# Performance work log

Hardware: AMD Instinct MI355X
Metric: run time of the kernel (lower is better)

## Reference

```python
import jax, jax.numpy as jnp
import numpy as np
from jax import lax

B, S, D, H, T = 128, 512, 128, 128, 20


def setup_inputs() -> dict:
    key = jax.random.key(0)
    ks = jax.random.split(key, 16)
    sc = 1.0 / np.sqrt(H)
    u = lambda k, shape: jax.random.uniform(k, shape, jnp.float32, -sc, sc)
    return {
        "inputs": jax.random.normal(ks[0], (B, S, D), jnp.float32),
        "tags": jax.random.randint(ks[1], (B, S), 0, T),
        "mask": jnp.ones((B, S), jnp.bool_),
        "w_ih_f": u(ks[2], (4 * H, D)),
        "w_hh_f": u(ks[3], (4 * H, H)),
        "b_f": u(ks[4], (4 * H,)),
        "w_ih_b": u(ks[5], (4 * H, D)),
        "w_hh_b": u(ks[6], (4 * H, H)),
        "b_b": u(ks[7], (4 * H,)),
        "w_out": u(ks[8], (T, 2 * H)),
        "b_out": u(ks[9], (T,)),
        "start_trans": jax.random.uniform(ks[10], (T,), jnp.float32, -0.1, 0.1),
        "end_trans": jax.random.uniform(ks[11], (T,), jnp.float32, -0.1, 0.1),
        "trans": jax.random.uniform(ks[12], (T, T), jnp.float32, -0.1, 0.1),
    }


def _lstm_dir(x, w_ih, w_hh, b, reverse):
    # x: [B,S,D] -> hidden states [B,S,H]
    xp = jnp.einsum('bsd,gd->bsg', x, w_ih) + b  # precomputed input gates [B,S,4H]
    if reverse:
        xp = xp[:, ::-1]
    h0 = jnp.zeros((x.shape[0], H), x.dtype)
    c0 = jnp.zeros((x.shape[0], H), x.dtype)

    def step(carry, xt):
        h, c = carry
        g = xt + h @ w_hh.T
        i, f, gg, o = jnp.split(g, 4, axis=-1)
        i, f, o = jax.nn.sigmoid(i), jax.nn.sigmoid(f), jax.nn.sigmoid(o)
        c = f * c + i * jnp.tanh(gg)
        h = o * jnp.tanh(c)
        return (h, c), h

    _, hs = lax.scan(step, (h0, c0), xp.transpose(1, 0, 2))
    hs = hs.transpose(1, 0, 2)  # [B,S,H]
    if reverse:
        hs = hs[:, ::-1]
    return hs


def _crf_nll(em, tags, mask, start_trans, end_trans, trans):
    # em: [B,S,T]; torchcrf log-likelihood, reduction='mean', negated
    b, s, t = em.shape
    maskf = mask.astype(em.dtype)
    batch = jnp.arange(b)
    # numerator: score of the gold path
    num = start_trans[tags[:, 0]] + em[batch, 0, tags[:, 0]]
    em_tag = jnp.take_along_axis(em, tags[:, :, None], axis=2)[:, :, 0]  # [B,S]
    trans_tag = trans[tags[:, :-1], tags[:, 1:]]  # [B,S-1]
    num = num + jnp.sum((trans_tag + em_tag[:, 1:]) * maskf[:, 1:], axis=1)
    seq_ends = jnp.sum(mask.astype(jnp.int32), axis=1) - 1
    num = num + end_trans[tags[batch, seq_ends]]
    # denominator: forward algorithm (logsumexp semiring) via scan
    score0 = start_trans[None, :] + em[:, 0]  # [B,T]

    def step(score, inp):
        em_t, m_t = inp
        nxt = jax.nn.logsumexp(score[:, :, None] + trans[None] + em_t[:, None, :], axis=1)
        return jnp.where(m_t[:, None], nxt, score), None

    score, _ = lax.scan(step, score0, (em[:, 1:].transpose(1, 0, 2), mask[:, 1:].T))
    den = jax.nn.logsumexp(score + end_trans[None, :], axis=1)
    return -jnp.mean(num - den)


def reference(inputs, tags, mask, w_ih_f, w_hh_f, b_f, w_ih_b, w_hh_b, b_b,
              w_out, b_out, start_trans, end_trans, trans):
    h_f = _lstm_dir(inputs, w_ih_f, w_hh_f, b_f, reverse=False)
    h_b = _lstm_dir(inputs, w_ih_b, w_hh_b, b_b, reverse=True)
    lstm_out = jnp.concatenate([h_f, h_b], axis=-1)  # [B,S,2H]
    emissions = jnp.einsum('bsh,th->bst', lstm_out, w_out) + b_out  # [B,S,T]
    return _crf_nll(emissions, tags, mask, start_trans, end_trans, trans)
```

## Files before the change

### kernel.cpp

```cpp
#include <hip/hip_runtime.h>
#include <cstdint>
#include <cstddef>

#define DEVINL __device__ __forceinline__

constexpr int Bz = 128, Sl = 512, Dm = 128, Hd = 128, NC = 1024, Tt = 20;
constexpr int Mrows = Bz * Sl;

constexpr size_t OFF_XP   = 17043456;
constexpr size_t OFF_HS   = 151261184;
constexpr size_t OFF_EM   = 184815616;
constexpr size_t OFF_PART = 190058496;

constexpr float LOG2E  = 1.4426950408889634f;
constexpr float LOG2E2 = 2.8853900817779268f;

DEVINL unsigned short f2bf(float f) {
    uint32_t u = __float_as_uint(f);
    u += 0x7fffu + ((u >> 16) & 1u);
    return (unsigned short)(u >> 16);
}
DEVINL float bf2f(unsigned short h) { return __uint_as_float(((uint32_t)h) << 16); }

DEVINL float rcpf(float x) { return __builtin_amdgcn_rcpf(x); }
DEVINL float exp2f_fast(float x) { return __builtin_amdgcn_exp2f(x); }

DEVINL void barrier_lds_only() {
    __asm__ __volatile__("s_waitcnt lgkmcnt(0)" ::: "memory");
    __builtin_amdgcn_s_barrier();
    __asm__ __volatile__("" ::: "memory");
}

typedef __attribute__((ext_vector_type(8))) __bf16 bf16x8;
typedef __attribute__((ext_vector_type(4))) float f32x4;
typedef _Float16 __attribute__((ext_vector_type(2))) half2_t;
typedef _Float16 __attribute__((ext_vector_type(8))) half8_t;

__global__ __launch_bounds__(256, 2) void gemm_xp_k(
    const float* __restrict__ X, const float* __restrict__ wihf, const float* __restrict__ wihb,
    const float* __restrict__ b_f, const float* __restrict__ b_b,
    unsigned short* __restrict__ xp)
{
    __shared__ __align__(16) unsigned short As[128 * 132];
    __shared__ __align__(16) unsigned short Bs[128 * 132];
    const int m0 = blockIdx.x * 128;
    const int tid = threadIdx.x;
    const int wave = tid >> 6, lane = tid & 63;
    const int wm = wave * 32;
    const int ln = lane & 15, qd = lane >> 4;
    const int colc = (tid & 31) * 4, rowb = tid >> 5;

    #pragma unroll
    for (int r = 0; r < 16; ++r) {
        int row = rowb + r * 8;
        float4 av = *(const float4*)(&X[(size_t)(m0 + row) * 128 + colc]);
        ushort4 au; au.x = f2bf(av.x); au.y = f2bf(av.y); au.z = f2bf(av.z); au.w = f2bf(av.w);
        *(ushort4*)(&As[row * 132 + colc]) = au;
    }

    const int bidx = m0 >> 9;
    const int tbase = m0 & 511;

    for (int nt = 0; nt < 8; ++nt) {
        const float* Bsrc = (nt < 4) ? (wihf + (size_t)nt * 128 * 128)
                                     : (wihb + (size_t)(nt - 4) * 128 * 128);
        __syncthreads();
        #pragma unroll
        for (int r = 0; r < 16; ++r) {
            int row = rowb + r * 8;
            float4 bv = *(const float4*)(&Bsrc[(size_t)row * 128 + colc]);
            ushort4 bu; bu.x = f2bf(bv.x); bu.y = f2bf(bv.y); bu.z = f2bf(bv.z); bu.w = f2bf(bv.w);
            *(ushort4*)(&Bs[row * 132 + colc]) = bu;
        }
        __syncthreads();

        f32x4 acc[2][8] = {};
        #pragma unroll
        for (int kk = 0; kk < 4; ++kk) {
            const int kb = kk * 32 + qd * 8;
            bf16x8 af[2], bfr[8];
            #pragma unroll
            for (int i = 0; i < 2; ++i)
                af[i] = *(const bf16x8*)(&As[(wm + i * 16 + ln) * 132 + kb]);
            #pragma unroll
            for (int j = 0; j < 8; ++j)
                bfr[j] = *(const bf16x8*)(&Bs[(j * 16 + ln) * 132 + kb]);
            #pragma unroll
            for (int i = 0; i < 2; ++i)
                #pragma unroll
                for (int j = 0; j < 8; ++j)
                    acc[i][j] = __builtin_amdgcn_mfma_f32_16x16x32_bf16(af[i], bfr[j], acc[i][j], 0, 0, 0);
        }
        #pragma unroll
        for (int j = 0; j < 8; ++j) {
            const int col = nt * 128 + j * 16 + ln;
            const float bv = (col < 512) ? b_f[col] : b_b[col - 512];
            const int gate = (col >> 7) & 3;
            const float sc = (gate == 2) ? LOG2E2 : LOG2E;
            #pragma unroll
            for (int i = 0; i < 2; ++i) {
                const int tloc = tbase + wm + i * 16 + qd * 4;
                ushort4 o;
                o.x = f2bf((acc[i][j][0] + bv) * sc); o.y = f2bf((acc[i][j][1] + bv) * sc);
                o.z = f2bf((acc[i][j][2] + bv) * sc); o.w = f2bf((acc[i][j][3] + bv) * sc);
                *(ushort4*)(xp + ((size_t)bidx * 1024 + col) * 512 + tloc) = o;
            }
        }
    }
}

__global__ __launch_bounds__(512, 1) void lstm_k(
    const float* __restrict__ whf, const float* __restrict__ whb,
    const unsigned short* __restrict__ xp, unsigned short* __restrict__ hs)
{
    __shared__ __align__(16) _Float16 h_buf[2][128];
    const int dir = blockIdx.x >> 7;
    const int b   = blockIdx.x & 127;
    const int tid = threadIdx.x;
    const int lane = tid & 63;
    const int wv   = tid >> 6;
    const int ln   = lane & 15;
    const int qd   = lane >> 4;
    const int u    = wv * 16 + ln;

    const float* wsrc = dir ? whb : whf;
    half8_t wfr[4][4];
    #pragma unroll
    for (int j = 0; j < 4; ++j) {
        const float sc = (j == 2) ? LOG2E2 : LOG2E;
        const float* wrow = wsrc + (size_t)(j * 128 + u) * 128;
        #pragma unroll
        for (int kk = 0; kk < 4; ++kk) {
            float4 v0 = *(const float4*)(wrow + kk * 32 + qd * 8);
            float4 v1 = *(const float4*)(wrow + kk * 32 + qd * 8 + 4);
            half8_t hv;
            hv[0] = (_Float16)(v0.x * sc); hv[1] = (_Float16)(v0.y * sc);
            hv[2] = (_Float16)(v0.z * sc); hv[3] = (_Float16)(v0.w * sc);
            hv[4] = (_Float16)(v1.x * sc); hv[5] = (_Float16)(v1.y * sc);
            hv[6] = (_Float16)(v1.z * sc); hv[7] = (_Float16)(v1.w * sc);
            wfr[j][kk] = hv;
        }
    }

    if (tid < 128) { h_buf[0][tid] = (_Float16)0.f; h_buf[1][tid] = (_Float16)0.f; }
    __syncthreads();

    const unsigned short* xr0 = xp + ((size_t)b * 1024 + (size_t)dir * 512 + u) * 512;
    const unsigned short* xr1 = xr0 + (size_t)128 * 512;
    const unsigned short* xr2 = xr0 + (size_t)256 * 512;
    const unsigned short* xr3 = xr0 + (size_t)384 * 512;

    unsigned short* hptr = hs + (size_t)dir * Mrows * 128 + (size_t)b * Sl * 128 + u
                              + (dir ? (size_t)(Sl - 1) * 128 : 0);
    const int hstep = dir ? -128 : 128;

    float c = 0.f;
    const f32x4 zc = {0.f, 0.f, 0.f, 0.f};
    ushort4 cur0, cur1, cur2, cur3;
    {
        const int o0 = dir ? 508 : 0;
        ushort4 r0 = *(const ushort4*)(xr0 + o0);
        ushort4 r1 = *(const ushort4*)(xr1 + o0);
        ushort4 r2 = *(const ushort4*)(xr2 + o0);
        ushort4 r3 = *(const ushort4*)(xr3 + o0);
        cur0 = dir ? ushort4{r0.w, r0.z, r0.y, r0.x} : r0;
        cur1 = dir ? ushort4{r1.w, r1.z, r1.y, r1.x} : r1;
        cur2 = dir ? ushort4{r2.w, r2.z, r2.y, r2.x} : r2;
        cur3 = dir ? ushort4{r3.w, r3.z, r3.y, r3.x} : r3;
    }

    for (int t = 0; t < Sl; t += 4) {
        #pragma unroll
        for (int j = 0; j < 4; ++j) {
            __asm__ __volatile__(""
                : "+v"(wfr[j][0]), "+v"(wfr[j][1]), "+v"(wfr[j][2]), "+v"(wfr[j][3]));
        }

        const int tn = (t + 4 < Sl) ? (t + 4) : 0;
        const int on = dir ? (508 - tn) : tn;
        ushort4 n0 = *(const ushort4*)(xr0 + on);
        ushort4 n1 = *(const ushort4*)(xr1 + on);
        ushort4 n2 = *(const ushort4*)(xr2 + on);
        ushort4 n3 = *(const ushort4*)(xr3 + on);

        #pragma unroll
        for (int s = 0; s < 4; ++s) {
            const int p = s & 1;
            const half8_t* hb = (const half8_t*)&h_buf[p][0];
            half8_t a0 = hb[qd];
            half8_t a1 = hb[4 + qd];
            half8_t a2 = hb[8 + qd];
            half8_t a3 = hb[12 + qd];

            f32x4 ac0, ac1, ac2, ac3;
            ac0 = __builtin_amdgcn_mfma_f32_16x16x32_f16(a0, wfr[0][0], zc, 0, 0, 0);
            ac1 = __builtin_amdgcn_mfma_f32_16x16x32_f16(a0, wfr[1][0], zc, 0, 0, 0);
            ac2 = __builtin_amdgcn_mfma_f32_16x16x32_f16(a0, wfr[2][0], zc, 0, 0, 0);
            ac3 = __builtin_amdgcn_mfma_f32_16x16x32_f16(a0, wfr[3][0], zc, 0, 0, 0);
            ac0 = __builtin_amdgcn_mfma_f32_16x16x32_f16(a1, wfr[0][1], ac0, 0, 0, 0);
            ac1 = __builtin_amdgcn_mfma_f32_16x16x32_f16(a1, wfr[1][1], ac1, 0, 0, 0);
            ac2 = __builtin_amdgcn_mfma_f32_16x16x32_f16(a1, wfr[2][1], ac2, 0, 0, 0);
            ac3 = __builtin_amdgcn_mfma_f32_16x16x32_f16(a1, wfr[3][1], ac3, 0, 0, 0);
            ac0 = __builtin_amdgcn_mfma_f32_16x16x32_f16(a2, wfr[0][2], ac0, 0, 0, 0);
            ac1 = __builtin_amdgcn_mfma_f32_16x16x32_f16(a2, wfr[1][2], ac1, 0, 0, 0);
            ac2 = __builtin_amdgcn_mfma_f32_16x16x32_f16(a2, wfr[2][2], ac2, 0, 0, 0);
            ac3 = __builtin_amdgcn_mfma_f32_16x16x32_f16(a2, wfr[3][2], ac3, 0, 0, 0);
            ac0 = __builtin_amdgcn_mfma_f32_16x16x32_f16(a3, wfr[0][3], ac0, 0, 0, 0);
            ac1 = __builtin_amdgcn_mfma_f32_16x16x32_f16(a3, wfr[1][3], ac1, 0, 0, 0);
            ac2 = __builtin_amdgcn_mfma_f32_16x16x32_f16(a3, wfr[2][3], ac2, 0, 0, 0);
            ac3 = __builtin_amdgcn_mfma_f32_16x16x32_f16(a3, wfr[3][3], ac3, 0, 0, 0);

            const unsigned short xb0 = (s == 0) ? cur0.x : (s == 1) ? cur0.y : (s == 2) ? cur0.z : cur0.w;
            const unsigned short xb1 = (s == 0) ? cur1.x : (s == 1) ? cur1.y : (s == 2) ? cur1.z : cur1.w;
            const unsigned short xb2 = (s == 0) ? cur2.x : (s == 1) ? cur2.y : (s == 2) ? cur2.z : cur2.w;
            const unsigned short xb3 = (s == 0) ? cur3.x : (s == 1) ? cur3.y : (s == 2) ? cur3.z : cur3.w;

            float t0 = ac0[0] + bf2f(xb0);
            float t1 = ac1[0] + bf2f(xb1);
            float t2 = ac2[0] + bf2f(xb2);
            float t3 = ac3[0] + bf2f(xb3);

            float gi = rcpf(1.f + exp2f_fast(-t0));
            float gf = rcpf(1.f + exp2f_fast(-t1));
            float gg = 2.f * rcpf(1.f + exp2f_fast(-t2)) - 1.f;
            float go = rcpf(1.f + exp2f_fast(-t3));
            c = fmaf(gf, c, gi * gg);
            float th = 1.f - 2.f * rcpf(1.f + exp2f_fast(LOG2E2 * c));
            float h = go * th;

            if (qd == 0) {
                _Float16 hh = (_Float16)h;
                h_buf[1 - p][u] = hh;
                unsigned short hbits; __builtin_memcpy(&hbits, &hh, 2);
                *hptr = hbits;
            }
            hptr += hstep;
            barrier_lds_only();
        }
        cur0 = dir ? ushort4{n0.w, n0.z, n0.y, n0.x} : n0;
        cur1 = dir ? ushort4{n1.w, n1.z, n1.y, n1.x} : n1;
        cur2 = dir ? ushort4{n2.w, n2.z, n2.y, n2.x} : n2;
        cur3 = dir ? ushort4{n3.w, n3.z, n3.y, n3.x} : n3;
    }
}

__global__ __launch_bounds__(320, 1) void emis_k(
    const unsigned short* __restrict__ hs, const float* __restrict__ wout,
    const float* __restrict__ bout, float* __restrict__ em)
{
    __shared__ __align__(16) half2_t wlds[20 * 128];
    const int b  = blockIdx.x >> 2;
    const int qt = blockIdx.x & 3;
    const int tid = threadIdx.x;

    #pragma unroll
    for (int k = 0; k < 8; ++k) {
        int i = tid + k * 320;
        wlds[i] = half2_t{(_Float16)wout[2 * i], (_Float16)wout[2 * i + 1]};
    }
    __syncthreads();

    const int tag  = tid % 20;
    const int copy = tid / 20;
    half2_t wreg[128];
    {
        const uint4* wl4 = (const uint4*)&wlds[tag * 128];
        #pragma unroll
        for (int k = 0; k < 32; ++k) {
            uint4 v = wl4[k];
            __builtin_memcpy(&wreg[4 * k], &v, 16);
        }
    }
    const float bo = bout[tag];
    const unsigned short* hf_base = hs + (size_t)b * Sl * 128;
    const unsigned short* hb_base = hs + (size_t)Mrows * 128 + (size_t)b * Sl * 128;

    #pragma unroll
    for (int i = 0; i < 8; ++i) {
        const int t = qt * 128 + copy + 16 * i;
        const uint4* hf4 = (const uint4*)(hf_base + (size_t)t * 128);
        const uint4* hb4 = (const uint4*)(hb_base + (size_t)t * 128);
        float a0 = bo, a1 = 0.f, a2 = 0.f, a3 = 0.f;
        #pragma unroll
        for (int k = 0; k < 16; ++k) {
            uint4 v = hf4[k];
            half2_t h2[4]; __builtin_memcpy(h2, &v, 16);
            a0 = __builtin_amdgcn_fdot2(wreg[4 * k + 0], h2[0], a0, false);
            a1 = __builtin_amdgcn_fdot2(wreg[4 * k + 1], h2[1], a1, false);
            a2 = __builtin_amdgcn_fdot2(wreg[4 * k + 2], h2[2], a2, false);
            a3 = __builtin_amdgcn_fdot2(wreg[4 * k + 3], h2[3], a3, false);
        }
        #pragma unroll
        for (int k = 0; k < 16; ++k) {
            uint4 v = hb4[k];
            half2_t h2[4]; __builtin_memcpy(h2, &v, 16);
            a0 = __builtin_amdgcn_fdot2(wreg[64 + 4 * k + 0], h2[0], a0, false);
            a1 = __builtin_amdgcn_fdot2(wreg[64 + 4 * k + 1], h2[1], a1, false);
            a2 = __builtin_amdgcn_fdot2(wreg[64 + 4 * k + 2], h2[2], a2, false);
            a3 = __builtin_amdgcn_fdot2(wreg[64 + 4 * k + 3], h2[3], a3, false);
        }
        em[((size_t)b * Sl + t) * Tt + tag] = (a0 + a1) + (a2 + a3);
    }
}

__global__ __launch_bounds__(64) void crf_k(
    const float* __restrict__ em, const int* __restrict__ tags,
    const float* __restrict__ st, const float* __restrict__ et,
    const float* __restrict__ trans, float* __restrict__ part)
{
    const int b = blockIdx.x, lane = threadIdx.x;
    const float* emb = em + (size_t)b * Sl * Tt;
    const int* tg = tags + (size_t)b * Sl;

    float nacc = 0.f;
    for (int t = 1 + lane; t < Sl; t += 64) {
        int tp = tg[t - 1], tc = tg[t];
        nacc += trans[tp * Tt + tc] + emb[t * Tt + tc];
    }
    #pragma unroll
    for (int off = 32; off; off >>= 1) nacc += __shfl_down(nacc, off);

    float Etr[20];
    #pragma unroll
    for (int i = 0; i < 20; ++i)
        Etr[i] = (lane < 20) ? __expf(trans[i * Tt + lane]) : 0.f;

    float C = 0.f;
    float p = (lane < 20) ? __expf(st[lane] + emb[lane]) : 0.f;

    float evr[8];
    #pragma unroll
    for (int s = 0; s < 8; ++s) {
        int tt = 1 + s; tt = tt < Sl ? tt : Sl - 1;
        evr[s] = (lane < 20) ? emb[(size_t)tt * Tt + lane] : 0.f;
    }

    for (int t0 = 1; t0 < Sl; t0 += 8) {
        #pragma unroll
        for (int s = 0; s < 8; ++s) {
            const int t = t0 + s;
            if (t < Sl) {
                float ev = evr[s];
                int tf = t + 8; tf = tf < Sl ? tf : Sl - 1;
                evr[s] = (lane < 20) ? emb[(size_t)tf * Tt + lane] : 0.f;

                float q0 = 0.f, q1 = 0.f, q2 = 0.f, q3 = 0.f;
                #pragma unroll
                for (int i = 0; i < 20; i += 4) {
                    q0 = fmaf(__int_as_float(__builtin_amdgcn_readlane(__float_as_int(p), i + 0)), Etr[i + 0], q0);
                    q1 = fmaf(__int_as_float(__builtin_amdgcn_readlane(__float_as_int(p), i + 1)), Etr[i + 1], q1);
                    q2 = fmaf(__int_as_float(__builtin_amdgcn_readlane(__float_as_int(p), i + 2)), Etr[i + 2], q2);
                    q3 = fmaf(__int_as_float(__builtin_amdgcn_readlane(__float_as_int(p), i + 3)), Etr[i + 3], q3);
                }
                p = ((q0 + q1) + (q2 + q3)) * __expf(ev);
                if ((s & 3) == 3) {
                    float S0 = 0.f, S1 = 0.f, S2 = 0.f, S3 = 0.f;
                    #pragma unroll
                    for (int i = 0; i < 20; i += 4) {
                        S0 += __int_as_float(__builtin_amdgcn_readlane(__float_as_int(p), i + 0));
                        S1 += __int_as_float(__builtin_amdgcn_readlane(__float_as_int(p), i + 1));
                        S2 += __int_as_float(__builtin_amdgcn_readlane(__float_as_int(p), i + 2));
                        S3 += __int_as_float(__builtin_amdgcn_readlane(__float_as_int(p), i + 3));
                    }
                    float Ssum = (S0 + S1) + (S2 + S3);
                    C += __logf(Ssum);
                    p *= rcpf(Ssum);
                }
            }
        }
    }
    float f = (lane < 20) ? p * __expf(et[lane]) : 0.f;
    float S0 = 0.f, S1 = 0.f, S2 = 0.f, S3 = 0.f;
    #pragma unroll
    for (int i = 0; i < 20; i += 4) {
        S0 += __int_as_float(__builtin_amdgcn_readlane(__float_as_int(f), i + 0));
        S1 += __int_as_float(__builtin_amdgcn_readlane(__float_as_int(f), i + 1));
        S2 += __int_as_float(__builtin_amdgcn_readlane(__float_as_int(f), i + 2));
        S3 += __int_as_float(__builtin_amdgcn_readlane(__float_as_int(f), i + 3));
    }
    float den = C + __logf((S0 + S1) + (S2 + S3));
    if (lane == 0)
        part[b] = nacc + st[tg[0]] + emb[tg[0]] + et[tg[Sl - 1]] - den;
}

__global__ void fin_k(const float* __restrict__ part, float* __restrict__ out) {
    int l = threadIdx.x;
    float v = part[l] + part[l + 64];
    #pragma unroll
    for (int off = 32; off; off >>= 1) v += __shfl_xor(v, off);
    if (l == 0) out[0] = -v * (1.f / 128.f);
}

extern "C" void kernel_launch(void* const* d_in, const int* in_sizes, int n_in,
                              void* d_out, int out_size, void* d_ws, size_t ws_size,
                              hipStream_t stream) {
    const float* x      = (const float*)d_in[0];
    const int*   tags   = (const int*)d_in[1];
    const float* w_ih_f = (const float*)d_in[3];
    const float* w_hh_f = (const float*)d_in[4];
    const float* b_f    = (const float*)d_in[5];
    const float* w_ih_b = (const float*)d_in[6];
    const float* w_hh_b = (const float*)d_in[7];
    const float* b_b    = (const float*)d_in[8];
    const float* w_out  = (const float*)d_in[9];
    const float* b_out  = (const float*)d_in[10];
    const float* st     = (const float*)d_in[11];
    const float* et     = (const float*)d_in[12];
    const float* trans  = (const float*)d_in[13];
    float* out = (float*)d_out;

    char* ws = (char*)d_ws;
    unsigned short* xp   = (unsigned short*)(ws + OFF_XP);
    unsigned short* hs   = (unsigned short*)(ws + OFF_HS);
    float*          em   = (float*)(ws + OFF_EM);
    float*          part = (float*)(ws + OFF_PART);

    gemm_xp_k<<<Mrows / 128, 256, 0, stream>>>(x, w_ih_f, w_ih_b, b_f, b_b, xp);
    lstm_k<<<256, 512, 0, stream>>>(w_hh_f, w_hh_b, xp, hs);
    emis_k<<<Bz * 4, 320, 0, stream>>>(hs, w_out, b_out, em);
    crf_k<<<Bz, 64, 0, stream>>>(em, tags, st, et, trans, part);
    fin_k<<<1, 64, 0, stream>>>(part, out);
}
```

Baseline: 496.6 us.

## Batch 16 sequences per LSTM block to fill MFMA rows

The recurrent LSTM kernel now processes 16 batch rows per block, using all 16 rows of each MFMA tile instead of one, so the grid shrinks from 256 to 16 blocks. Each lane handles four batch rows of gate math. The hidden state buffer in LDS is XOR-swizzled to avoid bank conflicts. This removes redundant MFMA work and weight-register loading per sequence, but it uses only 16 CUs and puts four times the per-step elementwise work and global traffic on each thread.

```diff
diff --git a/kernel.cpp b/kernel.cpp
--- a/kernel.cpp
+++ b/kernel.cpp
@@ -113,9 +113,9 @@
     const float* __restrict__ whf, const float* __restrict__ whb,
     const unsigned short* __restrict__ xp, unsigned short* __restrict__ hs)
 {
-    __shared__ __align__(16) _Float16 h_buf[2][128];
-    const int dir = blockIdx.x >> 7;
-    const int b   = blockIdx.x & 127;
+    __shared__ __align__(16) _Float16 h_buf[2][16][128];
+    const int dir = blockIdx.x >> 3;
+    const int b0  = (blockIdx.x & 7) << 4;
     const int tid = threadIdx.x;
     const int lane = tid & 63;
     const int wv   = tid >> 6;
@@ -142,31 +142,41 @@
         }
     }
 
-    if (tid < 128) { h_buf[0][tid] = (_Float16)0.f; h_buf[1][tid] = (_Float16)0.f; }
+    {
+        _Float16* hz = &h_buf[0][0][0];
+        #pragma unroll
+        for (int k = 0; k < 8; ++k) hz[tid + k * 512] = (_Float16)0.f;
+    }
     __syncthreads();
 
-    const unsigned short* xr0 = xp + ((size_t)b * 1024 + (size_t)dir * 512 + u) * 512;
-    const unsigned short* xr1 = xr0 + (size_t)128 * 512;
-    const unsigned short* xr2 = xr0 + (size_t)256 * 512;
-    const unsigned short* xr3 = xr0 + (size_t)384 * 512;
-
-    unsigned short* hptr = hs + (size_t)dir * Mrows * 128 + (size_t)b * Sl * 128 + u
-                              + (dir ? (size_t)(Sl - 1) * 128 : 0);
+    const unsigned short* xr[4][4];
+    #pragma unroll
+    for (int r = 0; r < 4; ++r)
+        #pragma unroll
+        for (int j = 0; j < 4; ++j)
+            xr[r][j] = xp + ((size_t)(b0 + 4 * qd + r) * 1024 + (size_t)dir * 512
+                             + (size_t)j * 128 + u) * 512;
+
+    unsigned short* hp[4];
+    #pragma unroll
+    for (int r = 0; r < 4; ++r)
+        hp[r] = hs + (size_t)dir * Mrows * 128 + (size_t)(b0 + 4 * qd + r) * Sl * 128 + u
+                   + (dir ? (size_t)(Sl - 1) * 128 : 0);
     const int hstep = dir ? -128 : 128;
 
-    float c = 0.f;
+    float cc0 = 0.f, cc1 = 0.f, cc2 = 0.f, cc3 = 0.f;
     const f32x4 zc = {0.f, 0.f, 0.f, 0.f};
-    ushort4 cur0, cur1, cur2, cur3;
+
+    ushort4 cur[4][4];
     {
         const int o0 = dir ? 508 : 0;
-        ushort4 r0 = *(const ushort4*)(xr0 + o0);
-        ushort4 r1 = *(const ushort4*)(xr1 + o0);
-        ushort4 r2 = *(const ushort4*)(xr2 + o0);
-        ushort4 r3 = *(const ushort4*)(xr3 + o0);
-        cur0 = dir ? ushort4{r0.w, r0.z, r0.y, r0.x} : r0;
-        cur1 = dir ? ushort4{r1.w, r1.z, r1.y, r1.x} : r1;
-        cur2 = dir ? ushort4{r2.w, r2.z, r2.y, r2.x} : r2;
-        cur3 = dir ? ushort4{r3.w, r3.z, r3.y, r3.x} : r3;
+        #pragma unroll
+        for (int r = 0; r < 4; ++r)
+            #pragma unroll
+            for (int j = 0; j < 4; ++j) {
+                ushort4 v = *(const ushort4*)(xr[r][j] + o0);
+                cur[r][j] = dir ? ushort4{v.w, v.z, v.y, v.x} : v;
+            }
     }
 
     for (int t = 0; t < Sl; t += 4) {
@@ -178,69 +188,84 @@
 
         const int tn = (t + 4 < Sl) ? (t + 4) : 0;
         const int on = dir ? (508 - tn) : tn;
-        ushort4 n0 = *(const ushort4*)(xr0 + on);
-        ushort4 n1 = *(const ushort4*)(xr1 + on);
-        ushort4 n2 = *(const ushort4*)(xr2 + on);
-        ushort4 n3 = *(const ushort4*)(xr3 + on);
+        ushort4 nxt[4][4];
+        #pragma unroll
+        for (int r = 0; r < 4; ++r)
+            #pragma unroll
+            for (int j = 0; j < 4; ++j)
+                nxt[r][j] = *(const ushort4*)(xr[r][j] + on);
 
         #pragma unroll
         for (int s = 0; s < 4; ++s) {
             const int p = s & 1;
-            const half8_t* hb = (const half8_t*)&h_buf[p][0];
-            half8_t a0 = hb[qd];
-            half8_t a1 = hb[4 + qd];
-            half8_t a2 = hb[8 + qd];
-            half8_t a3 = hb[12 + qd];
+
+            float xv[4][4];
+            #pragma unroll
+            for (int r = 0; r < 4; ++r)
+                #pragma unroll
+                for (int j = 0; j < 4; ++j) {
+                    const unsigned short xb =
+                        (s == 0) ? cur[r][j].x : (s == 1) ? cur[r][j].y
+                        : (s == 2) ? cur[r][j].z : cur[r][j].w;
+                    xv[r][j] = bf2f(xb);
+                }
+
+            half8_t a[4];
+            #pragma unroll
+            for (int kk = 0; kk < 4; ++kk) {
+                const int sg = (kk * 4 + qd) ^ (ln & 7);
+                a[kk] = *(const half8_t*)&h_buf[p][ln][sg * 8];
+            }
 
             f32x4 ac0, ac1, ac2, ac3;
-            ac0 = __builtin_amdgcn_mfma_f32_16x16x32_f16(a0, wfr[0][0], zc, 0, 0, 0);
-            ac1 = __builtin_amdgcn_mfma_f32_16x16x32_f16(a0, wfr[1][0], zc, 0, 0, 0);
-            ac2 = __builtin_amdgcn_mfma_f32_16x16x32_f16(a0, wfr[2][0], zc, 0, 0, 0);
-            ac3 = __builtin_amdgcn_mfma_f32_16x16x32_f16(a0, wfr[3][0], zc, 0, 0, 0);
-            ac0 = __builtin_amdgcn_mfma_f32_16x16x32_f16(a1, wfr[0][1], ac0, 0, 0, 0);
-            ac1 = __builtin_amdgcn_mfma_f32_16x16x32_f16(a1, wfr[1][1], ac1, 0, 0, 0);
-            ac2 = __builtin_amdgcn_mfma_f32_16x16x32_f16(a1, wfr[2][1], ac2, 0, 0, 0);
-            ac3 = __builtin_amdgcn_mfma_f32_16x16x32_f16(a1, wfr[3][1], ac3, 0, 0, 0);
-            ac0 = __builtin_amdgcn_mfma_f32_16x16x32_f16(a2, wfr[0][2], ac0, 0, 0, 0);
-            ac1 = __builtin_amdgcn_mfma_f32_16x16x32_f16(a2, wfr[1][2], ac1, 0, 0, 0);
-            ac2 = __builtin_amdgcn_mfma_f32_16x16x32_f16(a2, wfr[2][2], ac2, 0, 0, 0);
-            ac3 = __builtin_amdgcn_mfma_f32_16x16x32_f16(a2, wfr[3][2], ac3, 0, 0, 0);
-            ac0 = __builtin_amdgcn_mfma_f32_16x16x32_f16(a3, wfr[0][3], ac0, 0, 0, 0);
-            ac1 = __builtin_amdgcn_mfma_f32_16x16x32_f16(a3, wfr[1][3], ac1, 0, 0, 0);
-            ac2 = __builtin_amdgcn_mfma_f32_16x16x32_f16(a3, wfr[2][3], ac2, 0, 0, 0);
-            ac3 = __builtin_amdgcn_mfma_f32_16x16x32_f16(a3, wfr[3][3], ac3, 0, 0, 0);
-
-            const unsigned short xb0 = (s == 0) ? cur0.x : (s == 1) ? cur0.y : (s == 2) ? cur0.z : cur0.w;
-            const unsigned short xb1 = (s == 0) ? cur1.x : (s == 1) ? cur1.y : (s == 2) ? cur1.z : cur1.w;
-            const unsigned short xb2 = (s == 0) ? cur2.x : (s == 1) ? cur2.y : (s == 2) ? cur2.z : cur2.w;
-            const unsigned short xb3 = (s == 0) ? cur3.x : (s == 1) ? cur3.y : (s == 2) ? cur3.z : cur3.w;
-
-            float t0 = ac0[0] + bf2f(xb0);
-            float t1 = ac1[0] + bf2f(xb1);
-            float t2 = ac2[0] + bf2f(xb2);
-            float t3 = ac3[0] + bf2f(xb3);
-
-            float gi = rcpf(1.f + exp2f_fast(-t0));
-            float gf = rcpf(1.f + exp2f_fast(-t1));
-            float gg = 2.f * rcpf(1.f + exp2f_fast(-t2)) - 1.f;
-            float go = rcpf(1.f + exp2f_fast(-t3));
-            c = fmaf(gf, c, gi * gg);
-            float th = 1.f - 2.f * rcpf(1.f + exp2f_fast(LOG2E2 * c));
-            float h = go * th;
-
-            if (qd == 0) {
+            ac0 = __builtin_amdgcn_mfma_f32_16x16x32_f16(a[0], wfr[0][0], zc, 0, 0, 0);
+            ac1 = __builtin_amdgcn_mfma_f32_16x16x32_f16(a[0], wfr[1][0], zc, 0, 0, 0);
+            ac2 = __builtin_amdgcn_mfma_f32_16x16x32_f16(a[0], wfr[2][0], zc, 0, 0, 0);
+            ac3 = __builtin_amdgcn_mfma_f32_16x16x32_f16(a[0], wfr[3][0], zc, 0, 0, 0);
+            ac0 = __builtin_amdgcn_mfma_f32_16x16x32_f16(a[1], wfr[0][1], ac0, 0, 0, 0);
+            ac1 = __builtin_amdgcn_mfma_f32_16x16x32_f16(a[1], wfr[1][1], ac1, 0, 0, 0);
+            ac2 = __builtin_amdgcn_mfma_f32_16x16x32_f16(a[1], wfr[2][1], ac2, 0, 0, 0);
+            ac3 = __builtin_amdgcn_mfma_f32_16x16x32_f16(a[1], wfr[3][1], ac3, 0, 0, 0);
+            ac0 = __builtin_amdgcn_mfma_f32_16x16x32_f16(a[2], wfr[0][2], ac0, 0, 0, 0);
+            ac1 = __builtin_amdgcn_mfma_f32_16x16x32_f16(a[2], wfr[1][2], ac1, 0, 0, 0);
+            ac2 = __builtin_amdgcn_mfma_f32_16x16x32_f16(a[2], wfr[2][2], ac2, 0, 0, 0);
+            ac3 = __builtin_amdgcn_mfma_f32_16x16x32_f16(a[2], wfr[3][2], ac3, 0, 0, 0);
+            ac0 = __builtin_amdgcn_mfma_f32_16x16x32_f16(a[3], wfr[0][3], ac0, 0, 0, 0);
+            ac1 = __builtin_amdgcn_mfma_f32_16x16x32_f16(a[3], wfr[1][3], ac1, 0, 0, 0);
+            ac2 = __builtin_amdgcn_mfma_f32_16x16x32_f16(a[3], wfr[2][3], ac2, 0, 0, 0);
+            ac3 = __builtin_amdgcn_mfma_f32_16x16x32_f16(a[3], wfr[3][3], ac3, 0, 0, 0);
+
+            #pragma unroll
+            for (int r = 0; r < 4; ++r) {
+                float t0 = ac0[r] + xv[r][0];
+                float t1 = ac1[r] + xv[r][1];
+                float t2 = ac2[r] + xv[r][2];
+                float t3 = ac3[r] + xv[r][3];
+
+                float gi = rcpf(1.f + exp2f_fast(-t0));
+                float gf = rcpf(1.f + exp2f_fast(-t1));
+                float gg = 2.f * rcpf(1.f + exp2f_fast(-t2)) - 1.f;
+                float go = rcpf(1.f + exp2f_fast(-t3));
+                float& cc = (r == 0) ? cc0 : (r == 1) ? cc1 : (r == 2) ? cc2 : cc3;
+                cc = fmaf(gf, cc, gi * gg);
+                float th = 1.f - 2.f * rcpf(1.f + exp2f_fast(LOG2E2 * cc));
+                float h = go * th;
+
+                const int ch = 4 * qd + r;
                 _Float16 hh = (_Float16)h;
-                h_buf[1 - p][u] = hh;
+                h_buf[1 - p][ch][(((u >> 3) ^ (ch & 7)) << 3) | (u & 7)] = hh;
                 unsigned short hbits; __builtin_memcpy(&hbits, &hh, 2);
-                *hptr = hbits;
+                *hp[r] = hbits;
+                hp[r] += hstep;
             }
-            hptr += hstep;
             barrier_lds_only();
         }
-        cur0 = dir ? ushort4{n0.w, n0.z, n0.y, n0.x} : n0;
-        cur1 = dir ? ushort4{n1.w, n1.z, n1.y, n1.x} : n1;
-        cur2 = dir ? ushort4{n2.w, n2.z, n2.y, n2.x} : n2;
-        cur3 = dir ? ushort4{n3.w, n3.z, n3.y, n3.x} : n3;
+        #pragma unroll
+        for (int r = 0; r < 4; ++r)
+            #pragma unroll
+            for (int j = 0; j < 4; ++j)
+                cur[r][j] = dir ? ushort4{nxt[r][j].w, nxt[r][j].z, nxt[r][j].y, nxt[r][j].x}
+                                : nxt[r][j];
     }
 }
 
@@ -416,7 +441,7 @@
     float*          part = (float*)(ws + OFF_PART);
 
     gemm_xp_k<<<Mrows / 128, 256, 0, stream>>>(x, w_ih_f, w_ih_b, b_f, b_b, xp);
-    lstm_k<<<256, 512, 0, stream>>>(w_hh_f, w_hh_b, xp, hs);
+    lstm_k<<<16, 512, 0, stream>>>(w_hh_f, w_hh_b, xp, hs);
     emis_k<<<Bz * 4, 320, 0, stream>>>(hs, w_out, b_out, em);
     crf_k<<<Bz, 64, 0, stream>>>(em, tags, st, et, trans, part);
     fin_k<<<1, 64, 0, stream>>>(part, out);
```

Result: slower. 1.291 ms (+160.1%).
